# Kernel tuning notes

Measured on AMD Instinct MI355X. Metric: run time of the kernel, lower is better.

## Reference

```python
import jax, jax.numpy as jnp
import numpy as np

NUM_BINS = 256
BN_EPS = 1e-5


def setup_inputs() -> dict:
    key = jax.random.key(0)
    ks = jax.random.split(key, 16)
    B, C, H, W = 16, 64, 256, 256
    x = jax.random.uniform(ks[0], (B, C, H, W), dtype=jnp.float32) * 255.0
    return {
        "x": x,
        "conv1_w": jax.random.normal(ks[1], (C, C), dtype=jnp.float32) * 0.05,
        "conv1_b": jax.random.normal(ks[2], (C,), dtype=jnp.float32) * 0.05,
        "bn1_gamma": jax.random.uniform(ks[3], (C,), dtype=jnp.float32) + 0.5,
        "bn1_beta": jax.random.normal(ks[4], (C,), dtype=jnp.float32) * 0.05,
        "bn1_mean": jax.random.normal(ks[5], (C,), dtype=jnp.float32) * 0.05,
        "bn1_var": jax.random.uniform(ks[6], (C,), dtype=jnp.float32) + 0.5,
        "conv2_w": jax.random.normal(ks[7], (1, C), dtype=jnp.float32) * 0.05,
        "conv2_b": jax.random.normal(ks[8], (1,), dtype=jnp.float32) * 0.05,
        "bn2_gamma": jax.random.uniform(ks[9], (1,), dtype=jnp.float32) + 0.5,
        "bn2_beta": jax.random.normal(ks[10], (1,), dtype=jnp.float32) * 0.05,
        "bn2_mean": jax.random.normal(ks[11], (1,), dtype=jnp.float32) * 0.05,
        "bn2_var": jax.random.uniform(ks[12], (1,), dtype=jnp.float32) + 0.5,
    }


def _histc_argmax(x):
    # Replicates torch.histc(v, bins=NUM_BINS, min=0, max=255) per (b, c)
    # followed by argmax over bins. Out-of-range values are ignored by histc.
    B, C, H, W = x.shape
    flat = x.reshape(B * C, H * W)
    in_range = (flat >= 0.0) & (flat <= 255.0)
    # histc bin index: floor((v - min) * bins / (max - min)); v == max -> last bin
    idx = jnp.clip((flat * (NUM_BINS / 255.0)).astype(jnp.int32), 0, NUM_BINS - 1)
    rows = jnp.arange(B * C)[:, None]
    hist = jnp.zeros((B * C, NUM_BINS), dtype=jnp.float32).at[rows, idx].add(
        in_range.astype(jnp.float32)
    )
    return hist.argmax(axis=-1).reshape(B, C)  # [B, C] dominant bin indices


def _bn(a, gamma, beta, mean, var):
    inv = gamma * jax.lax.rsqrt(var + BN_EPS)
    return a * inv[None, :, None, None] + (beta - mean * inv)[None, :, None, None]


def reference(x, conv1_w, conv1_b, bn1_gamma, bn1_beta, bn1_mean, bn1_var,
              conv2_w, conv2_b, bn2_gamma, bn2_beta, bn2_mean, bn2_var):
    bin_size = 256 // NUM_BINS  # == 1 for default num_bins
    dominant = _histc_argmax(x)  # [B, C]
    # per-pixel bin index: torch's x.float() // bin_size then .long()
    pixel_bins = jnp.floor(x / bin_size).astype(jnp.int32)  # [B, C, H, W]
    att = (pixel_bins != dominant[:, :, None, None]).astype(x.dtype)
    # conv1 (1x1) -> bn1 -> relu
    a = jnp.einsum('bchw,oc->bohw', att, conv1_w) + conv1_b[None, :, None, None]
    a = jax.nn.relu(_bn(a, bn1_gamma, bn1_beta, bn1_mean, bn1_var))
    # conv2 (1x1, C->1) -> bn2 -> sigmoid
    a = jnp.einsum('bchw,oc->bohw', a, conv2_w) + conv2_b[None, :, None, None]
    a = jax.nn.sigmoid(_bn(a, bn2_gamma, bn2_beta, bn2_mean, bn2_var))
    return x * a
```

## Files before the change

kernel.cpp:

```cpp
#include <hip/hip_runtime.h>
#include <stdint.h>

#define CCH 64
#define HWPIX 65536
#define NBINS 256

typedef float f4 __attribute__((ext_vector_type(4)));

#define GLDS16(gp, lp)                                                        \
    __builtin_amdgcn_global_load_lds(                                         \
        (const __attribute__((address_space(1))) uint32_t*)(gp),              \
        (__attribute__((address_space(3))) uint32_t*)(lp), 16, 0, 0)


__global__ __launch_bounds__(64) void precomp_kernel(
    const float* __restrict__ w1, const float* __restrict__ b1,
    const float* __restrict__ g1, const float* __restrict__ be1,
    const float* __restrict__ m1, const float* __restrict__ v1,
    const float* __restrict__ w2, const float* __restrict__ b2,
    const float* __restrict__ g2, const float* __restrict__ be2,
    const float* __restrict__ m2, const float* __restrict__ v2,
    float* __restrict__ ws)
{
    int o = threadIdx.x;
    float inv1 = g1[o] * rsqrtf(v1[o] + 1e-5f);
    float S = 0.f;
    for (int c = 0; c < CCH; ++c) S += w1[o * CCH + c];
    float beta1p = be1[o] - m1[o] * inv1;
    float base_pre = (S + b1[o]) * inv1 + beta1p;
    for (int c = 0; c < CCH; ++c) ws[1024 + o * CCH + c] = w1[o * CCH + c] * inv1;
    ws[5120 + o] = base_pre;
    float w2o = w2[o];
    ws[5184 + o] = w2o;
    float t = fmaxf(base_pre, 0.f) * w2o;
    #pragma unroll
    for (int off = 32; off > 0; off >>= 1) t += __shfl_down(t, off, 64);
    if (o == 0) {
        float inv2 = g2[0] * rsqrtf(v2[0] + 1e-5f);
        float beta2p = be2[0] - m2[0] * inv2;
        float z = (t + b2[0]) * inv2 + beta2p;
        ws[5248] = inv2;
        ws[5249] = beta2p;
        ws[5250] = b2[0];
        ws[5251] = 1.f / (1.f + expf(-z));
    }
    __syncthreads();
    {
        int c = o;
        float t1 = 0.f;
        for (int oo = 0; oo < CCH; ++oo) {
            float acc = ws[5120 + oo] - ws[1024 + oo * CCH + c];
            t1 += fmaxf(acc, 0.f) * ws[5184 + oo];
        }
        float z = (t1 + ws[5250]) * ws[5248] + ws[5249];
        ws[5312 + c] = 1.f / (1.f + expf(-z));
    }
}

__global__ __launch_bounds__(64) void precomp2_kernel(float* __restrict__ ws)
{
    int c1 = blockIdx.x, c2 = threadIdx.x;
    float t = 0.f;
    for (int o = 0; o < CCH; ++o) {
        float acc = ws[5120 + o] - ws[1024 + o * CCH + c1] - ws[1024 + o * CCH + c2];
        t += fmaxf(acc, 0.f) * ws[5184 + o];
    }
    float z = (t + ws[5250]) * ws[5248] + ws[5249];
    ws[8192 + c1 * CCH + c2] = 1.f / (1.f + expf(-z));
}

__global__ __launch_bounds__(256) void hist_kernel(
    const float* __restrict__ x, int* __restrict__ dom)
{
    __shared__ unsigned h[32][NBINS + 1];
    __shared__ unsigned long long red[NBINS];
    int tid = threadIdx.x;
    const float4* xp = (const float4*)(x + (size_t)blockIdx.x * HWPIX);

    for (int i = tid; i < 32 * (NBINS + 1); i += 256) ((unsigned*)h)[i] = 0;
    __syncthreads();

    unsigned* hmine = h[tid >> 3];
    const float scale = 256.0f / 255.0f;
    #pragma unroll 4
    for (int t = 0; t < HWPIX / 4 / 256; ++t) {
        float4 v = xp[t * 256 + tid];
        float vv[4] = {v.x, v.y, v.z, v.w};
        #pragma unroll
        for (int j = 0; j < 4; ++j) {
            float f = vv[j];
            if (f >= 0.f && f <= 255.f) {
                int bi = (int)(f * scale);
                bi = bi > NBINS - 1 ? NBINS - 1 : bi;
                atomicAdd(&hmine[bi], 1u);
            }
        }
    }
    __syncthreads();

    unsigned cnt = 0;
    #pragma unroll
    for (int k = 0; k < 32; ++k) cnt += h[k][tid];
    red[tid] = ((unsigned long long)cnt << 32) | (unsigned)(NBINS - 1 - tid);
    __syncthreads();
    #pragma unroll
    for (int s = 128; s > 0; s >>= 1) {
        if (tid < s) {
            unsigned long long a = red[tid], b = red[tid + s];
            red[tid] = a > b ? a : b;
        }
        __syncthreads();
    }
    if (tid == 0) dom[blockIdx.x] = (NBINS - 1) - (int)(red[0] & 0xffffffffu);
}

__global__ __launch_bounds__(256, 8) void main_kernel(
    const float* __restrict__ x, const float* __restrict__ ws,
    const int* __restrict__ dom, float* __restrict__ out)
{
    __shared__ __align__(16) float tile[CCH * 64];
    __shared__ unsigned pm[4][CCH];
    __shared__ float ss[CCH];
    __shared__ float df[CCH];

    int tid = threadIdx.x;
    int b = blockIdx.x >> 10;
    int p04 = (blockIdx.x & 1023) << 4;

    if (tid < CCH) df[tid] = (float)dom[b * CCH + tid];

    const f4* xb4 = (const f4*)(x + ((size_t)b << 22));
    #pragma unroll
    for (int k = 0; k < 4; ++k) {
        int id = (k << 8) + tid;
        int c = id >> 4, col = id & 15;
        GLDS16(xb4 + ((size_t)c << 14) + p04 + col, tile + (id << 2));
    }
    __syncthreads();

    {
        int part = tid >> 6, px = tid & 63;
        unsigned mloc = 0;
        #pragma unroll
        for (int cc = 0; cc < 16; ++cc) {
            int c = (part << 4) | cc;
            float v = tile[(c << 6) | px];
            float d = df[c];
            mloc |= (unsigned)(v >= d && v < d + 1.0f) << cc;
        }
        pm[part][px] = mloc;
    }
    __syncthreads();

    if (tid < CCH) {
        int px = tid;
        unsigned long long m = (unsigned long long)pm[0][px]
            | ((unsigned long long)pm[1][px] << 16)
            | ((unsigned long long)pm[2][px] << 32)
            | ((unsigned long long)pm[3][px] << 48);
        float s;
        if (m == 0ull) {
            s = ws[5251];
        } else {
            int c1 = __builtin_ctzll(m);
            unsigned long long r1 = m & (m - 1);
            if (r1 == 0ull) {
                s = ws[5312 + c1];
            } else {
                int c2 = __builtin_ctzll(r1);
                unsigned long long r2 = r1 & (r1 - 1);
                if (r2 == 0ull) {
                    s = ws[8192 + (c1 << 6) + c2];
                } else {
                    float t = 0.f;
                    for (int o = 0; o < CCH; ++o) {
                        float acc = ws[5120 + o];
                        unsigned long long mm = m;
                        const float* row = ws + 1024 + (o << 6);
                        while (mm) {
                            int c = __builtin_ctzll(mm);
                            mm &= mm - 1;
                            acc -= row[c];
                        }
                        t += fmaxf(acc, 0.f) * ws[5184 + o];
                    }
                    float z = (t + ws[5250]) * ws[5248] + ws[5249];
                    s = 1.f / (1.f + expf(-z));
                }
            }
        }
        ss[px] = s;
    }
    __syncthreads();

    f4* ob4 = (f4*)(out + ((size_t)b << 22));
    #pragma unroll
    for (int k = 0; k < 4; ++k) {
        int id = (k << 8) + tid;
        int c = id >> 4, col = id & 15;
        f4 v = *(const f4*)&tile[id << 2];
        f4 sv = *(const f4*)&ss[col << 2];
        v *= sv;
        __builtin_nontemporal_store(v, &ob4[((size_t)c << 14) + p04 + col]);
    }
}

extern "C" void kernel_launch(void* const* d_in, const int* in_sizes, int n_in,
                              void* d_out, int out_size, void* d_ws, size_t ws_size,
                              hipStream_t stream) {
    const float* x   = (const float*)d_in[0];
    const float* w1  = (const float*)d_in[1];
    const float* b1  = (const float*)d_in[2];
    const float* g1  = (const float*)d_in[3];
    const float* be1 = (const float*)d_in[4];
    const float* m1  = (const float*)d_in[5];
    const float* v1  = (const float*)d_in[6];
    const float* w2  = (const float*)d_in[7];
    const float* b2  = (const float*)d_in[8];
    const float* g2  = (const float*)d_in[9];
    const float* be2 = (const float*)d_in[10];
    const float* m2  = (const float*)d_in[11];
    const float* v2  = (const float*)d_in[12];

    float* ws  = (float*)d_ws;
    int*   dom = (int*)d_ws;
    float* outp = (float*)d_out;

    int B = in_sizes[0] / (CCH * HWPIX);

    precomp_kernel<<<1, 64, 0, stream>>>(w1, b1, g1, be1, m1, v1,
                                         w2, b2, g2, be2, m2, v2, ws);
    precomp2_kernel<<<CCH, 64, 0, stream>>>(ws);
    hist_kernel<<<B * CCH, 256, 0, stream>>>(x, dom);
    main_kernel<<<B * (HWPIX / 64), 256, 0, stream>>>(x, ws, dom, outp);
}
```

Measured before the change: 168.2 us.

## Fuse histogram and attention passes into one cooperative kernel with per-batch counters

Merges the histogram/argmax kernel and the main attention kernel into a single cooperative launch. Each block first builds one channel's histogram, publishes its dominant bin and bumps a per-batch atomic counter, then spins until all 64 channels of its batch are done. After that it loops over 16 pixel tiles of that batch. The aim is to drop a launch boundary and to re-read x while the batch's data may still be in cache. In exchange, the 1024 resident blocks each process their tiles one at a time with barriers, which may cut memory parallelism. The histogram also uses fewer sub-histograms, which raises LDS atomic contention.

```diff
diff --git a/kernel.cpp b/kernel.cpp
--- a/kernel.cpp
+++ b/kernel.cpp
@@ -23,6 +23,7 @@
     float* __restrict__ ws)
 {
     int o = threadIdx.x;
+    if (o < 16) ((int*)ws)[5400 + o] = 0;
     float inv1 = g1[o] * rsqrtf(v1[o] + 1e-5f);
     float S = 0.f;
     for (int c = 0; c < CCH; ++c) S += w1[o * CCH + c];
@@ -69,139 +70,161 @@
     ws[8192 + c1 * CCH + c2] = 1.f / (1.f + expf(-z));
 }
 
-__global__ __launch_bounds__(256) void hist_kernel(
-    const float* __restrict__ x, int* __restrict__ dom)
+__global__ __launch_bounds__(256, 8) void fused_kernel(
+    const float* __restrict__ x, float* __restrict__ ws, float* __restrict__ out)
 {
-    __shared__ unsigned h[32][NBINS + 1];
-    __shared__ unsigned long long red[NBINS];
+    __shared__ __align__(16) unsigned char smem[18496];
     int tid = threadIdx.x;
-    const float4* xp = (const float4*)(x + (size_t)blockIdx.x * HWPIX);
-
-    for (int i = tid; i < 32 * (NBINS + 1); i += 256) ((unsigned*)h)[i] = 0;
+    int g = blockIdx.x >> 6;
+    int r = blockIdx.x & 63;
+    int bc = g * CCH + r;
+
+    int* domp = (int*)ws;
+    int* cntp = (int*)ws + 5400;
+
+    {
+        unsigned (*h)[NBINS + 1] = (unsigned(*)[NBINS + 1])smem;
+        unsigned long long* red = (unsigned long long*)(smem + 16448);
+        const float4* xp = (const float4*)(x + (size_t)bc * HWPIX);
+
+        for (int i = tid; i < 16 * (NBINS + 1); i += 256) ((unsigned*)h)[i] = 0;
+        __syncthreads();
+
+        unsigned* hmine = h[tid >> 4];
+        const float scale = 256.0f / 255.0f;
+        #pragma unroll 4
+        for (int t = 0; t < HWPIX / 4 / 256; ++t) {
+            float4 v = xp[t * 256 + tid];
+            float vv[4] = {v.x, v.y, v.z, v.w};
+            #pragma unroll
+            for (int j = 0; j < 4; ++j) {
+                float f = vv[j];
+                if (f >= 0.f && f <= 255.f) {
+                    int bi = (int)(f * scale);
+                    bi = bi > NBINS - 1 ? NBINS - 1 : bi;
+                    atomicAdd(&hmine[bi], 1u);
+                }
+            }
+        }
+        __syncthreads();
+
+        unsigned cnt = 0;
+        #pragma unroll
+        for (int k = 0; k < 16; ++k) cnt += h[k][tid];
+        red[tid] = ((unsigned long long)cnt << 32) | (unsigned)(NBINS - 1 - tid);
+        __syncthreads();
+        #pragma unroll
+        for (int s = 128; s > 0; s >>= 1) {
+            if (tid < s) {
+                unsigned long long a = red[tid], b2 = red[tid + s];
+                red[tid] = a > b2 ? a : b2;
+            }
+            __syncthreads();
+        }
+        if (tid == 0) {
+            int dval = (NBINS - 1) - (int)(red[0] & 0xffffffffu);
+            __hip_atomic_store(&domp[bc], dval, __ATOMIC_RELAXED,
+                               __HIP_MEMORY_SCOPE_AGENT);
+            __hip_atomic_fetch_add(&cntp[g], 1, __ATOMIC_RELEASE,
+                                   __HIP_MEMORY_SCOPE_AGENT);
+        }
+    }
+
+    if (tid == 0) {
+        while (__hip_atomic_load(&cntp[g], __ATOMIC_ACQUIRE,
+                                 __HIP_MEMORY_SCOPE_AGENT) < CCH)
+            __builtin_amdgcn_s_sleep(16);
+    }
     __syncthreads();
 
-    unsigned* hmine = h[tid >> 3];
-    const float scale = 256.0f / 255.0f;
-    #pragma unroll 4
-    for (int t = 0; t < HWPIX / 4 / 256; ++t) {
-        float4 v = xp[t * 256 + tid];
-        float vv[4] = {v.x, v.y, v.z, v.w};
-        #pragma unroll
-        for (int j = 0; j < 4; ++j) {
-            float f = vv[j];
-            if (f >= 0.f && f <= 255.f) {
-                int bi = (int)(f * scale);
-                bi = bi > NBINS - 1 ? NBINS - 1 : bi;
-                atomicAdd(&hmine[bi], 1u);
-            }
-        }
-    }
+    float*    tile = (float*)smem;
+    float*    ss   = (float*)(smem + 16384);
+    float*    df   = (float*)(smem + 16640);
+    unsigned* pm   = (unsigned*)(smem + 16896);
+
+    if (tid < CCH)
+        df[tid] = (float)__hip_atomic_load(&domp[g * CCH + tid], __ATOMIC_RELAXED,
+                                           __HIP_MEMORY_SCOPE_AGENT);
     __syncthreads();
 
-    unsigned cnt = 0;
-    #pragma unroll
-    for (int k = 0; k < 32; ++k) cnt += h[k][tid];
-    red[tid] = ((unsigned long long)cnt << 32) | (unsigned)(NBINS - 1 - tid);
-    __syncthreads();
-    #pragma unroll
-    for (int s = 128; s > 0; s >>= 1) {
-        if (tid < s) {
-            unsigned long long a = red[tid], b = red[tid + s];
-            red[tid] = a > b ? a : b;
-        }
-        __syncthreads();
-    }
-    if (tid == 0) dom[blockIdx.x] = (NBINS - 1) - (int)(red[0] & 0xffffffffu);
-}
-
-__global__ __launch_bounds__(256, 8) void main_kernel(
-    const float* __restrict__ x, const float* __restrict__ ws,
-    const int* __restrict__ dom, float* __restrict__ out)
-{
-    __shared__ __align__(16) float tile[CCH * 64];
-    __shared__ unsigned pm[4][CCH];
-    __shared__ float ss[CCH];
-    __shared__ float df[CCH];
-
-    int tid = threadIdx.x;
-    int b = blockIdx.x >> 10;
-    int p04 = (blockIdx.x & 1023) << 4;
-
-    if (tid < CCH) df[tid] = (float)dom[b * CCH + tid];
-
-    const f4* xb4 = (const f4*)(x + ((size_t)b << 22));
-    #pragma unroll
-    for (int k = 0; k < 4; ++k) {
-        int id = (k << 8) + tid;
-        int c = id >> 4, col = id & 15;
-        GLDS16(xb4 + ((size_t)c << 14) + p04 + col, tile + (id << 2));
-    }
-    __syncthreads();
-
-    {
-        int part = tid >> 6, px = tid & 63;
-        unsigned mloc = 0;
-        #pragma unroll
-        for (int cc = 0; cc < 16; ++cc) {
-            int c = (part << 4) | cc;
-            float v = tile[(c << 6) | px];
-            float d = df[c];
-            mloc |= (unsigned)(v >= d && v < d + 1.0f) << cc;
-        }
-        pm[part][px] = mloc;
-    }
-    __syncthreads();
-
-    if (tid < CCH) {
-        int px = tid;
-        unsigned long long m = (unsigned long long)pm[0][px]
-            | ((unsigned long long)pm[1][px] << 16)
-            | ((unsigned long long)pm[2][px] << 32)
-            | ((unsigned long long)pm[3][px] << 48);
-        float s;
-        if (m == 0ull) {
-            s = ws[5251];
-        } else {
-            int c1 = __builtin_ctzll(m);
-            unsigned long long r1 = m & (m - 1);
-            if (r1 == 0ull) {
-                s = ws[5312 + c1];
+    const f4* xb4 = (const f4*)(x + ((size_t)g << 22));
+    f4*       ob4 = (f4*)(out + ((size_t)g << 22));
+
+    for (int jj = 0; jj < 16; ++jj) {
+        int j = (r << 4) + jj;
+        #pragma unroll
+        for (int k = 0; k < 4; ++k) {
+            int id = (k << 8) + tid;
+            int c = id >> 4, col = id & 15;
+            GLDS16(xb4 + ((size_t)c << 14) + (j << 4) + col, tile + (id << 2));
+        }
+        __syncthreads();
+
+        {
+            int part = tid >> 6, px = tid & 63;
+            unsigned mloc = 0;
+            #pragma unroll
+            for (int cc = 0; cc < 16; ++cc) {
+                int c = (part << 4) | cc;
+                float v = tile[(c << 6) | px];
+                float d = df[c];
+                mloc |= (unsigned)(v >= d && v < d + 1.0f) << cc;
+            }
+            pm[(part << 6) | px] = mloc;
+        }
+        __syncthreads();
+
+        if (tid < CCH) {
+            int px = tid;
+            unsigned long long m = (unsigned long long)pm[px]
+                | ((unsigned long long)pm[64 + px] << 16)
+                | ((unsigned long long)pm[128 + px] << 32)
+                | ((unsigned long long)pm[192 + px] << 48);
+            float s;
+            if (m == 0ull) {
+                s = ws[5251];
             } else {
-                int c2 = __builtin_ctzll(r1);
-                unsigned long long r2 = r1 & (r1 - 1);
-                if (r2 == 0ull) {
-                    s = ws[8192 + (c1 << 6) + c2];
+                int c1 = __builtin_ctzll(m);
+                unsigned long long r1 = m & (m - 1);
+                if (r1 == 0ull) {
+                    s = ws[5312 + c1];
                 } else {
-                    float t = 0.f;
-                    for (int o = 0; o < CCH; ++o) {
-                        float acc = ws[5120 + o];
-                        unsigned long long mm = m;
-                        const float* row = ws + 1024 + (o << 6);
-                        while (mm) {
-                            int c = __builtin_ctzll(mm);
-                            mm &= mm - 1;
-                            acc -= row[c];
+                    int c2 = __builtin_ctzll(r1);
+                    unsigned long long r2 = r1 & (r1 - 1);
+                    if (r2 == 0ull) {
+                        s = ws[8192 + (c1 << 6) + c2];
+                    } else {
+                        float t = 0.f;
+                        for (int o = 0; o < CCH; ++o) {
+                            float acc = ws[5120 + o];
+                            unsigned long long mm = m;
+                            const float* row = ws + 1024 + (o << 6);
+                            while (mm) {
+                                int c = __builtin_ctzll(mm);
+                                mm &= mm - 1;
+                                acc -= row[c];
+                            }
+                            t += fmaxf(acc, 0.f) * ws[5184 + o];
                         }
-                        t += fmaxf(acc, 0.f) * ws[5184 + o];
+                        float z = (t + ws[5250]) * ws[5248] + ws[5249];
+                        s = 1.f / (1.f + expf(-z));
                     }
-                    float z = (t + ws[5250]) * ws[5248] + ws[5249];
-                    s = 1.f / (1.f + expf(-z));
                 }
             }
-        }
-        ss[px] = s;
-    }
-    __syncthreads();
-
-    f4* ob4 = (f4*)(out + ((size_t)b << 22));
-    #pragma unroll
-    for (int k = 0; k < 4; ++k) {
-        int id = (k << 8) + tid;
-        int c = id >> 4, col = id & 15;
-        f4 v = *(const f4*)&tile[id << 2];
-        f4 sv = *(const f4*)&ss[col << 2];
-        v *= sv;
-        __builtin_nontemporal_store(v, &ob4[((size_t)c << 14) + p04 + col]);
+            ss[px] = s;
+        }
+        __syncthreads();
+
+        #pragma unroll
+        for (int k = 0; k < 4; ++k) {
+            int id = (k << 8) + tid;
+            int c = id >> 4, col = id & 15;
+            f4 v = *(const f4*)&tile[id << 2];
+            f4 sv = *(const f4*)&ss[col << 2];
+            v *= sv;
+            __builtin_nontemporal_store(v, &ob4[((size_t)c << 14) + (j << 4) + col]);
+        }
+        __syncthreads();
     }
 }
 
@@ -223,7 +246,6 @@
     const float* v2  = (const float*)d_in[12];
 
     float* ws  = (float*)d_ws;
-    int*   dom = (int*)d_ws;
     float* outp = (float*)d_out;
 
     int B = in_sizes[0] / (CCH * HWPIX);
@@ -231,6 +253,8 @@
     precomp_kernel<<<1, 64, 0, stream>>>(w1, b1, g1, be1, m1, v1,
                                          w2, b2, g2, be2, m2, v2, ws);
     precomp2_kernel<<<CCH, 64, 0, stream>>>(ws);
-    hist_kernel<<<B * CCH, 256, 0, stream>>>(x, dom);
-    main_kernel<<<B * (HWPIX / 64), 256, 0, stream>>>(x, ws, dom, outp);
-}
+
+    void* args[] = { (void*)&x, (void*)&ws, (void*)&outp };
+    hipLaunchCooperativeKernel((void*)fused_kernel, dim3(B * CCH), dim3(256),
+                               args, 0, stream);
+}
```

New measurement: 380.4 us. 126% more time.
